# Kernel tuning notes

Measured on AMD Instinct MI355X. Metric: run time of the kernel, lower is better.

## Reference

```python
import jax, jax.numpy as jnp
import numpy as np

N = 100_000
E = 1_600_000
F_IN = 14
H = 64
N_BLOCKS = 105
N_STEMS_OUT = 105
S = 10_000
KEEP = 0.8  # 1 - drop_prob


def setup_inputs() -> dict:
    key = jax.random.key(0)
    ks = jax.random.split(key, 16)
    x = jax.random.normal(ks[0], (N, F_IN), dtype=jnp.float32)
    edge_index = jax.random.randint(ks[1], (2, E), 0, N, dtype=jnp.int64)
    stem_idxs = jax.random.randint(ks[2], (S,), 0, N, dtype=jnp.int64)
    # learned params (glorot-ish init)
    W1 = jax.random.normal(ks[3], (F_IN + 1, H), dtype=jnp.float32) / np.sqrt(F_IN + 1)
    b1 = jnp.zeros((H,), dtype=jnp.float32)
    W2 = jax.random.normal(ks[4], (H, H), dtype=jnp.float32) / np.sqrt(H)
    b2 = jnp.zeros((H,), dtype=jnp.float32)
    Wb = jax.random.normal(ks[5], (H, N_BLOCKS), dtype=jnp.float32) / np.sqrt(H)
    bb = jnp.zeros((N_BLOCKS,), dtype=jnp.float32)
    Ws = jax.random.normal(ks[6], (H, N_STEMS_OUT), dtype=jnp.float32) / np.sqrt(H)
    bs = jnp.zeros((N_STEMS_OUT,), dtype=jnp.float32)
    # inverted-dropout masks (deterministic reference for F.dropout(p=0.2))
    drop1 = (jax.random.bernoulli(ks[7], KEEP, (N, H)).astype(jnp.float32)) / KEEP
    drop2 = (jax.random.bernoulli(ks[8], KEEP, (N, H)).astype(jnp.float32)) / KEEP
    # gumbel noise g = -log(-log(U)) for gumbel_softmax(tau=1, hard=False)
    u1 = jax.random.uniform(ks[9], (N, N_BLOCKS), minval=1e-10, maxval=1.0)
    u2 = jax.random.uniform(ks[10], (N, N_STEMS_OUT), minval=1e-10, maxval=1.0)
    gb = -jnp.log(-jnp.log(u1)).astype(jnp.float32)
    gs = -jnp.log(-jnp.log(u2)).astype(jnp.float32)
    return {"x": x, "W1": W1, "b1": b1, "W2": W2, "b2": b2,
            "Wb": Wb, "bb": bb, "Ws": Ws, "bs": bs,
            "drop1": drop1, "drop2": drop2, "gb": gb, "gs": gs,
            "edge_index": edge_index, "stem_idxs": stem_idxs}


def gcn_conv(x, W, b, src, dst, norm, n):
    """PyG GCNConv (normalize=True, self-loops already appended in src/dst/norm)."""
    xw = x @ W                                    # [n, out]
    msg = xw[src] * norm[:, None]                 # gather + scale  [E+n, out]
    out = jax.ops.segment_sum(msg, dst, num_segments=n)  # scatter-add
    return out + b


def _gcn_norm(edge_index, n):
    # append self loops, edge weight 1; symmetric normalization
    loops = jnp.arange(n, dtype=edge_index.dtype)
    src = jnp.concatenate([edge_index[0], loops])
    dst = jnp.concatenate([edge_index[1], loops])
    deg = jax.ops.segment_sum(jnp.ones_like(dst, dtype=jnp.float32), dst, num_segments=n)
    dis = jnp.where(deg > 0, jax.lax.rsqrt(deg), 0.0)
    norm = dis[src] * dis[dst]
    return src, dst, norm


def reference(x, W1, b1, W2, b2, Wb, bb, Ws, bs, drop1, drop2, gb, gs, edge_index, stem_idxs):
    n = x.shape[0]
    stem_feature = jnp.zeros((n,), dtype=x.dtype).at[stem_idxs].set(1.0)
    h = jnp.concatenate([x, stem_feature[:, None]], axis=1)  # [N, F_IN+1]
    src, dst, norm = _gcn_norm(edge_index, n)
    h = jax.nn.relu(gcn_conv(h, W1, b1, src, dst, norm, n)) * drop1
    h = jax.nn.relu(gcn_conv(h, W2, b2, src, dst, norm, n)) * drop2
    block_logits = h @ Wb + bb
    stem_logits = h @ Ws + bs
    selected_block = jax.nn.softmax(block_logits + gb, axis=-1)  # gumbel_softmax tau=1 soft
    selected_stem = jax.nn.softmax(stem_logits + gs, axis=-1)
    return (block_logits, stem_logits, selected_block, selected_stem)
```

## Files before the change

kernel.cpp:

```cpp
#include <hip/hip_runtime.h>
#include <hip/hip_bf16.h>
#include <math.h>

#define N_NODES 100000
#define N_EDGES 1600000
#define FIN 14
#define H 64
#define NB 105
#define S_CNT 10000
#define SCAN_BLOCKS 391
#define NBKT 391
#define BBLK 250
#define EPB 6400

__global__ __launch_bounds__(256) void deg_kernel(const int* __restrict__ dst,
                                                  int* __restrict__ deg) {
    int e = blockIdx.x * 256 + threadIdx.x;
    atomicAdd(&deg[dst[e]], 1);
}

__global__ __launch_bounds__(256) void stem_kernel(const int* __restrict__ idx,
                                                   float* __restrict__ stem01) {
    int i = blockIdx.x * 256 + threadIdx.x;
    if (i < S_CNT) stem01[idx[i]] = 1.0f;
}

__global__ __launch_bounds__(256) void dis_kernel(const int* __restrict__ deg,
                                                  float* __restrict__ dis) {
    int i = blockIdx.x * 256 + threadIdx.x;
    if (i < N_NODES) dis[i] = rsqrtf((float)deg[i] + 1.0f);
}

__global__ __launch_bounds__(256) void scan1_kernel(const int* __restrict__ deg,
                                                    int* __restrict__ rowptr,
                                                    int* __restrict__ bsum) {
    __shared__ int s[256];
    int t = threadIdx.x;
    int i = blockIdx.x * 256 + t;
    int v = (i < N_NODES) ? deg[i] : 0;
    s[t] = v;
    __syncthreads();
#pragma unroll
    for (int o = 1; o < 256; o <<= 1) {
        int x = (t >= o) ? s[t - o] : 0;
        __syncthreads();
        s[t] += x;
        __syncthreads();
    }
    if (i < N_NODES) rowptr[i + 1] = s[t];
    if (t == 255) bsum[blockIdx.x] = s[255];
}

__global__ __launch_bounds__(512) void scan2_kernel(const int* __restrict__ bsum,
                                                    int* __restrict__ boff) {
    __shared__ int s[512];
    int t = threadIdx.x;
    int v = (t < SCAN_BLOCKS) ? bsum[t] : 0;
    s[t] = v;
    __syncthreads();
#pragma unroll
    for (int o = 1; o < 512; o <<= 1) {
        int x = (t >= o) ? s[t - o] : 0;
        __syncthreads();
        s[t] += x;
        __syncthreads();
    }
    if (t < SCAN_BLOCKS) boff[t] = s[t] - v;
}

__global__ __launch_bounds__(256) void scan3_kernel(const int* __restrict__ boff,
                                                    int* __restrict__ rowptr) {
    int t = threadIdx.x;
    int i = blockIdx.x * 256 + t;
    if (i < N_NODES) rowptr[i + 1] += boff[blockIdx.x];
    if (i == 0) rowptr[0] = 0;
}

__global__ __launch_bounds__(256) void bincnt_kernel(const int* __restrict__ dst,
                                                     int* __restrict__ hist) {
    __shared__ int lh[NBKT];
    int t = threadIdx.x;
    for (int i = t; i < NBKT; i += 256) lh[i] = 0;
    __syncthreads();
    int e0 = blockIdx.x * EPB;
    for (int i = t; i < EPB; i += 256) atomicAdd(&lh[dst[e0 + i] >> 8], 1);
    __syncthreads();
    for (int i = t; i < NBKT; i += 256) hist[i * BBLK + blockIdx.x] = lh[i];
}

__global__ __launch_bounds__(256) void binscan_kernel(int* __restrict__ hist,
                                                      const int* __restrict__ rowptr) {
    __shared__ int s[256];
    int t = threadIdx.x, b = blockIdx.x;
    int v = (t < BBLK) ? hist[b * BBLK + t] : 0;
    s[t] = v;
    __syncthreads();
#pragma unroll
    for (int o = 1; o < 256; o <<= 1) {
        int x = (t >= o) ? s[t - o] : 0;
        __syncthreads();
        s[t] += x;
        __syncthreads();
    }
    if (t < BBLK) hist[b * BBLK + t] = rowptr[b * 256] + s[t] - v;
}

__global__ __launch_bounds__(256) void binscat_kernel(const int* __restrict__ src,
                                                      const int* __restrict__ dst,
                                                      const int* __restrict__ hist,
                                                      int* __restrict__ tmp) {
    __shared__ int lofs[NBKT];
    __shared__ int lcnt[NBKT];
    int t = threadIdx.x;
    for (int i = t; i < NBKT; i += 256) {
        lofs[i] = hist[i * BBLK + blockIdx.x];
        lcnt[i] = 0;
    }
    __syncthreads();
    int e0 = blockIdx.x * EPB;
    for (int i = t; i < EPB; i += 256) {
        int s = src[e0 + i], d = dst[e0 + i];
        int b = d >> 8;
        int r = atomicAdd(&lcnt[b], 1);
        tmp[lofs[b] + r] = s | ((d & 255) << 17);
    }
}

__global__ __launch_bounds__(256) void bsort_kernel(const int* __restrict__ tmp,
                                                    const int* __restrict__ rowptr,
                                                    int* __restrict__ col) {
    __shared__ int cur[256];
    int t = threadIdx.x, b = blockIdx.x;
    int n0 = b * 256;
    int idx = n0 + t;
    cur[t] = (idx < N_NODES) ? rowptr[idx] : 0;
    __syncthreads();
    int beg = rowptr[n0];
    int nend = n0 + 256; if (nend > N_NODES) nend = N_NODES;
    int end = rowptr[nend];
    for (int i = beg + t; i < end; i += 256) {
        int p = tmp[i];
        int pos = atomicAdd(&cur[p >> 17], 1);
        col[pos] = p & 0x1FFFF;
    }
}

__global__ __launch_bounds__(256) void wpadT_kernel(const float* __restrict__ Wb,
                                                    const float* __restrict__ Ws,
                                                    float* __restrict__ WpT) {
    int i = blockIdx.x * 256 + threadIdx.x;
    if (i < 224 * 64) {
        int c = i >> 6, k = i & 63;
        float w = 0.f;
        if (c < NB) w = Wb[k * NB + c];
        else if (c >= 112 && c < 112 + NB) w = Ws[k * NB + (c - 112)];
        WpT[i] = w;
    }
}

__global__ __launch_bounds__(256) void xw1_kernel(const float* __restrict__ x,
                                                  const float* __restrict__ stem01,
                                                  const float* __restrict__ dis,
                                                  const float* __restrict__ W1,
                                                  float* __restrict__ xws) {
    __shared__ __align__(16) float W1s[15 * 64];
    __shared__ __align__(16) float xs[4][16];
    int tid = threadIdx.x;
    for (int i = tid; i < 960; i += 256) W1s[i] = W1[i];
    int n0 = blockIdx.x * 4;
    if (tid < 60) {
        int r = tid / 15, k = tid % 15;
        int n = n0 + r;
        xs[r][k] = (k < FIN) ? x[n * FIN + k] : stem01[n];
    }
    __syncthreads();
    int r = tid >> 6, f = tid & 63;
    float acc = 0.f;
#pragma unroll
    for (int k = 0; k < 15; k++) acc += xs[r][k] * W1s[k * 64 + f];
    xws[(n0 + r) * 64 + f] = acc * dis[n0 + r];
}

__global__ __launch_bounds__(256) void agg_csr_kernel(const float* __restrict__ xws,
                                                      const int* __restrict__ rowptr,
                                                      const int* __restrict__ col,
                                                      const float* __restrict__ dis,
                                                      const float* __restrict__ bias,
                                                      const float* __restrict__ drop,
                                                      float* __restrict__ hout) {
    int node = (blockIdx.x * 256 + threadIdx.x) >> 6;
    int f = threadIdx.x & 63;
    int beg = rowptr[node], end = rowptr[node + 1];
    float acc0 = xws[node * 64 + f];
    float acc1 = 0.f, acc2 = 0.f, acc3 = 0.f;
    int j = beg;
    for (; j + 4 <= end; j += 4) {
        int s0 = col[j], s1 = col[j + 1], s2 = col[j + 2], s3 = col[j + 3];
        acc0 += xws[s0 * 64 + f];
        acc1 += xws[s1 * 64 + f];
        acc2 += xws[s2 * 64 + f];
        acc3 += xws[s3 * 64 + f];
    }
    for (; j < end; j++) acc0 += xws[col[j] * 64 + f];
    float acc = (acc0 + acc1) + (acc2 + acc3);
    float r = fmaxf(fmaf(dis[node], acc, bias[f]), 0.f) * drop[node * 64 + f];
    hout[node * 64 + f] = r;
}

__global__ __launch_bounds__(256) void xw2_kernel(const float* __restrict__ h,
                                                  const float* __restrict__ dis,
                                                  const float* __restrict__ W2,
                                                  float* __restrict__ xws) {
    __shared__ __align__(16) float W2s[64 * 64];
    __shared__ __align__(16) float hsT[64 * 68];
    int tid = threadIdx.x;
    for (int i = tid; i < 4096; i += 256) W2s[i] = W2[i];
    int n0 = blockIdx.x * 64;
    for (int i = tid; i < 4096; i += 256) {
        int m = i >> 6, k = i & 63;
        int n = n0 + m;
        hsT[k * 68 + m] = (n < N_NODES) ? h[n * 64 + k] : 0.f;
    }
    __syncthreads();
    int fg = tid & 15, mg = tid >> 4;
    int f0 = fg * 4, m0 = mg * 4;
    float acc[4][4];
#pragma unroll
    for (int i = 0; i < 4; i++)
#pragma unroll
        for (int j = 0; j < 4; j++) acc[i][j] = 0.f;
    for (int k = 0; k < 64; k++) {
        float4 w = *(const float4*)&W2s[k * 64 + f0];
        float4 hv = *(const float4*)&hsT[k * 68 + m0];
        float hh[4] = {hv.x, hv.y, hv.z, hv.w};
#pragma unroll
        for (int i = 0; i < 4; i++) {
            acc[i][0] += hh[i] * w.x;
            acc[i][1] += hh[i] * w.y;
            acc[i][2] += hh[i] * w.z;
            acc[i][3] += hh[i] * w.w;
        }
    }
#pragma unroll
    for (int i = 0; i < 4; i++) {
        int n = n0 + m0 + i;
        if (n < N_NODES) {
            float ds = dis[n];
            float4 r = make_float4(acc[i][0] * ds, acc[i][1] * ds,
                                   acc[i][2] * ds, acc[i][3] * ds);
            *(float4*)&xws[n * 64 + f0] = r;
        }
    }
}

__global__ __launch_bounds__(256) void hlog_kernel(const float* __restrict__ h2,
                                                   const float* __restrict__ WpT,
                                                   const float* __restrict__ bb,
                                                   const float* __restrict__ bs,
                                                   float* __restrict__ out) {
    __shared__ __align__(16) float hl[4][8 * 64];
    const size_t NA = (size_t)N_NODES * NB;
    int tid = threadIdx.x;
    int widx = tid >> 6, lane = tid & 63;
    int wid = blockIdx.x * 4 + widx;
    int n0 = wid * 8;
    int half = lane >> 5;
    int lp = lane & 31;

    {
        const float4* src = (const float4*)(h2 + (size_t)n0 * 64);
        float4* dstp = (float4*)hl[widx];
        dstp[lane] = src[lane];
        dstp[64 + lane] = src[64 + lane];
    }

    int hoff = half * 112;
    const float* bias = half ? bs : bb;
    bool v3 = (lp + 96) < NB;
    int c3 = v3 ? (lp + 96) : 104;
    const float* w0p = WpT + (size_t)(hoff + lp) * 64;
    const float* w1p = WpT + (size_t)(hoff + lp + 32) * 64;
    const float* w2p = WpT + (size_t)(hoff + lp + 64) * 64;
    const float* w3p = WpT + (size_t)(hoff + c3) * 64;
    float bv0 = bias[lp], bv1 = bias[lp + 32], bv2 = bias[lp + 64];
    float bv3 = v3 ? bias[lp + 96] : 0.f;

    float acc[8][4];
#pragma unroll
    for (int j = 0; j < 8; j++)
#pragma unroll
        for (int r = 0; r < 4; r++) acc[j][r] = 0.f;

    const float* hw = hl[widx];
#pragma unroll 4
    for (int k4 = 0; k4 < 16; k4++) {
        float4 w0 = *(const float4*)&w0p[k4 * 4];
        float4 w1 = *(const float4*)&w1p[k4 * 4];
        float4 w2 = *(const float4*)&w2p[k4 * 4];
        float4 w3 = *(const float4*)&w3p[k4 * 4];
#pragma unroll
        for (int j = 0; j < 8; j++) {
            float4 hq = *(const float4*)&hw[j * 64 + k4 * 4];
            acc[j][0] += hq.x * w0.x + hq.y * w0.y + hq.z * w0.z + hq.w * w0.w;
            acc[j][1] += hq.x * w1.x + hq.y * w1.y + hq.z * w1.z + hq.w * w1.w;
            acc[j][2] += hq.x * w2.x + hq.y * w2.y + hq.z * w2.z + hq.w * w2.w;
            acc[j][3] += hq.x * w3.x + hq.y * w3.y + hq.z * w3.z + hq.w * w3.w;
        }
    }

    float* ob = out + (size_t)half * NA + (size_t)n0 * NB;
#pragma unroll
    for (int j = 0; j < 8; j++) {
        float* lo = ob + (size_t)j * NB;
        lo[lp] = acc[j][0] + bv0;
        lo[lp + 32] = acc[j][1] + bv1;
        lo[lp + 64] = acc[j][2] + bv2;
        if (v3) lo[lp + 96] = acc[j][3] + bv3;
    }
}

__global__ __launch_bounds__(256) void gsm_kernel(const float* __restrict__ gb,
                                                  const float* __restrict__ gs,
                                                  float* __restrict__ out) {
    const size_t NA = (size_t)N_NODES * NB;
    int wid = blockIdx.x * 4 + (threadIdx.x >> 6);
    int lane = threadIdx.x & 63;
    int n = wid >> 1;
    if (n >= N_NODES) return;
    int head = wid & 1;
    const float* L = out + (head ? NA : 0) + (size_t)n * NB;
    const float* g = (head ? gs : gb) + (size_t)n * NB;
    float z0 = L[lane] + g[lane];
    float z1 = (lane < NB - 64) ? L[lane + 64] + g[lane + 64] : -INFINITY;
    float m = fmaxf(z0, z1);
#pragma unroll
    for (int off = 32; off; off >>= 1) m = fmaxf(m, __shfl_xor(m, off));
    float e0 = __expf(z0 - m);
    float e1 = (lane < NB - 64) ? __expf(z1 - m) : 0.f;
    float s = e0 + e1;
#pragma unroll
    for (int off = 32; off; off >>= 1) s += __shfl_xor(s, off);
    float inv = 1.f / s;
    float* o = out + (2 + head) * NA + (size_t)n * NB;
    o[lane] = e0 * inv;
    if (lane < NB - 64) o[lane + 64] = e1 * inv;
}

extern "C" void kernel_launch(void* const* d_in, const int* in_sizes, int n_in,
                              void* d_out, int out_size, void* d_ws, size_t ws_size,
                              hipStream_t stream) {
    const float* x     = (const float*)d_in[0];
    const float* W1    = (const float*)d_in[1];
    const float* b1    = (const float*)d_in[2];
    const float* W2    = (const float*)d_in[3];
    const float* b2    = (const float*)d_in[4];
    const float* Wb    = (const float*)d_in[5];
    const float* bb    = (const float*)d_in[6];
    const float* Ws    = (const float*)d_in[7];
    const float* bs    = (const float*)d_in[8];
    const float* drop1 = (const float*)d_in[9];
    const float* drop2 = (const float*)d_in[10];
    const float* gb    = (const float*)d_in[11];
    const float* gs    = (const float*)d_in[12];
    const int* edge    = (const int*)d_in[13];
    const int* stem    = (const int*)d_in[14];
    float* out = (float*)d_out;

    float* A      = (float*)d_ws;
    float* B      = A + (size_t)N_NODES * 64;
    float* dis    = B + (size_t)N_NODES * 64;
    float* stem01 = dis + N_NODES;
    int*   deg    = (int*)(stem01 + N_NODES);
    int*   rowptr = deg + N_NODES;
    int*   hist   = rowptr + (N_NODES + 1);
    int*   bsum   = hist + N_NODES;
    int*   boff   = bsum + SCAN_BLOCKS;
    int*   col    = boff + SCAN_BLOCKS;
    float* WpT    = (float*)(col + N_EDGES);
    int*   tmp    = (int*)d_out;

    const int* esrc = edge;
    const int* edst = edge + N_EDGES;

    hipMemsetAsync(deg, 0, N_NODES * sizeof(int), stream);
    hipMemsetAsync(stem01, 0, N_NODES * sizeof(float), stream);

    deg_kernel<<<N_EDGES / 256, 256, 0, stream>>>(edst, deg);
    stem_kernel<<<(S_CNT + 255) / 256, 256, 0, stream>>>(stem, stem01);
    dis_kernel<<<SCAN_BLOCKS, 256, 0, stream>>>(deg, dis);
    wpadT_kernel<<<(224 * 64 + 255) / 256, 256, 0, stream>>>(Wb, Ws, WpT);

    scan1_kernel<<<SCAN_BLOCKS, 256, 0, stream>>>(deg, rowptr, bsum);
    scan2_kernel<<<1, 512, 0, stream>>>(bsum, boff);
    scan3_kernel<<<SCAN_BLOCKS, 256, 0, stream>>>(boff, rowptr);

    bincnt_kernel<<<BBLK, 256, 0, stream>>>(edst, hist);
    binscan_kernel<<<NBKT, 256, 0, stream>>>(hist, rowptr);
    binscat_kernel<<<BBLK, 256, 0, stream>>>(esrc, edst, hist, tmp);
    bsort_kernel<<<NBKT, 256, 0, stream>>>(tmp, rowptr, col);

    xw1_kernel<<<N_NODES / 4, 256, 0, stream>>>(x, stem01, dis, W1, A);
    agg_csr_kernel<<<(N_NODES * 64) / 256, 256, 0, stream>>>(A, rowptr, col, dis, b1, drop1, B);

    xw2_kernel<<<(N_NODES + 63) / 64, 256, 0, stream>>>(B, dis, W2, B);
    agg_csr_kernel<<<(N_NODES * 64) / 256, 256, 0, stream>>>(B, rowptr, col, dis, b2, drop2, A);

    hlog_kernel<<<N_NODES / 8 / 4, 256, 0, stream>>>(A, WpT, bb, bs, out);
    gsm_kernel<<<(2 * N_NODES) / 4, 256, 0, stream>>>(gb, gs, out);
}
```

Measured before the change: 729.4 us.

## Fuse logits GEMM with gumbel softmax, staging swizzled weights in LDS

Merges the output-head GEMM kernel and the gumbel-softmax kernel into one kernel that computes the logits, adds the bias and gumbel noise, and does the row softmax in registers. This removes the round trip of reading the logits back from global memory and one kernel launch. Each block now handles a single head (grid y = 2). It loads that head's padded weight matrix into shared memory with an XOR swizzle to avoid bank conflicts, instead of reading weights from global memory per lane. The cost is that every block reloads about 28KB of weights into LDS, and the node tile in LDS is staged twice, once per head.

```diff
diff --git a/kernel.cpp b/kernel.cpp
--- a/kernel.cpp
+++ b/kernel.cpp
@@ -253,19 +253,30 @@
     }
 }
 
-__global__ __launch_bounds__(256) void hlog_kernel(const float* __restrict__ h2,
-                                                   const float* __restrict__ WpT,
-                                                   const float* __restrict__ bb,
-                                                   const float* __restrict__ bs,
-                                                   float* __restrict__ out) {
+__global__ __launch_bounds__(256) void fh2_kernel(const float* __restrict__ h2,
+                                                  const float* __restrict__ WpT,
+                                                  const float* __restrict__ bb,
+                                                  const float* __restrict__ bs,
+                                                  const float* __restrict__ gb,
+                                                  const float* __restrict__ gs,
+                                                  float* __restrict__ out) {
+    __shared__ __align__(16) float Wl[112 * 64];
     __shared__ __align__(16) float hl[4][8 * 64];
     const size_t NA = (size_t)N_NODES * NB;
     int tid = threadIdx.x;
+    int head = blockIdx.y;
+
+    {
+        const float4* wsrc = (const float4*)(WpT + (size_t)head * 112 * 64);
+        for (int i = tid; i < 112 * 16; i += 256) {
+            int c = i >> 4, ch = i & 15;
+            float4 v = wsrc[i];
+            *(float4*)&Wl[(c << 6) + ((ch ^ (c & 15)) << 2)] = v;
+        }
+    }
+
     int widx = tid >> 6, lane = tid & 63;
-    int wid = blockIdx.x * 4 + widx;
-    int n0 = wid * 8;
-    int half = lane >> 5;
-    int lp = lane & 31;
+    int n0 = (blockIdx.x * 4 + widx) * 8;
 
     {
         const float4* src = (const float4*)(h2 + (size_t)n0 * 64);
@@ -273,77 +284,58 @@
         dstp[lane] = src[lane];
         dstp[64 + lane] = src[64 + lane];
     }
-
-    int hoff = half * 112;
-    const float* bias = half ? bs : bb;
-    bool v3 = (lp + 96) < NB;
-    int c3 = v3 ? (lp + 96) : 104;
-    const float* w0p = WpT + (size_t)(hoff + lp) * 64;
-    const float* w1p = WpT + (size_t)(hoff + lp + 32) * 64;
-    const float* w2p = WpT + (size_t)(hoff + lp + 64) * 64;
-    const float* w3p = WpT + (size_t)(hoff + c3) * 64;
-    float bv0 = bias[lp], bv1 = bias[lp + 32], bv2 = bias[lp + 64];
-    float bv3 = v3 ? bias[lp + 96] : 0.f;
-
-    float acc[8][4];
-#pragma unroll
-    for (int j = 0; j < 8; j++)
-#pragma unroll
-        for (int r = 0; r < 4; r++) acc[j][r] = 0.f;
+    __syncthreads();
+
+    float acc[8][2];
+#pragma unroll
+    for (int j = 0; j < 8; j++) { acc[j][0] = 0.f; acc[j][1] = 0.f; }
 
     const float* hw = hl[widx];
+    int sw = lane & 15;
+    int b0 = lane << 6;
+    int b1 = (lane + 64) << 6;
 #pragma unroll 4
     for (int k4 = 0; k4 < 16; k4++) {
-        float4 w0 = *(const float4*)&w0p[k4 * 4];
-        float4 w1 = *(const float4*)&w1p[k4 * 4];
-        float4 w2 = *(const float4*)&w2p[k4 * 4];
-        float4 w3 = *(const float4*)&w3p[k4 * 4];
+        int wo = (k4 ^ sw) << 2;
+        float4 w0 = *(const float4*)&Wl[b0 + wo];
+        float4 w1 = *(const float4*)&Wl[b1 + wo];
 #pragma unroll
         for (int j = 0; j < 8; j++) {
-            float4 hq = *(const float4*)&hw[j * 64 + k4 * 4];
+            float4 hq = *(const float4*)&hw[(j << 6) + (k4 << 2)];
             acc[j][0] += hq.x * w0.x + hq.y * w0.y + hq.z * w0.z + hq.w * w0.w;
             acc[j][1] += hq.x * w1.x + hq.y * w1.y + hq.z * w1.z + hq.w * w1.w;
-            acc[j][2] += hq.x * w2.x + hq.y * w2.y + hq.z * w2.z + hq.w * w2.w;
-            acc[j][3] += hq.x * w3.x + hq.y * w3.y + hq.z * w3.z + hq.w * w3.w;
         }
     }
 
-    float* ob = out + (size_t)half * NA + (size_t)n0 * NB;
+    bool v1 = lane < (NB - 64);
+    const float* bias = head ? bs : bb;
+    const float* g = head ? gs : gb;
+    float bv0 = bias[lane];
+    float bv1 = v1 ? bias[lane + 64] : 0.f;
+    float* obase = out + (size_t)head * NA;
 #pragma unroll
     for (int j = 0; j < 8; j++) {
-        float* lo = ob + (size_t)j * NB;
-        lo[lp] = acc[j][0] + bv0;
-        lo[lp + 32] = acc[j][1] + bv1;
-        lo[lp + 64] = acc[j][2] + bv2;
-        if (v3) lo[lp + 96] = acc[j][3] + bv3;
-    }
-}
-
-__global__ __launch_bounds__(256) void gsm_kernel(const float* __restrict__ gb,
-                                                  const float* __restrict__ gs,
-                                                  float* __restrict__ out) {
-    const size_t NA = (size_t)N_NODES * NB;
-    int wid = blockIdx.x * 4 + (threadIdx.x >> 6);
-    int lane = threadIdx.x & 63;
-    int n = wid >> 1;
-    if (n >= N_NODES) return;
-    int head = wid & 1;
-    const float* L = out + (head ? NA : 0) + (size_t)n * NB;
-    const float* g = (head ? gs : gb) + (size_t)n * NB;
-    float z0 = L[lane] + g[lane];
-    float z1 = (lane < NB - 64) ? L[lane + 64] + g[lane + 64] : -INFINITY;
-    float m = fmaxf(z0, z1);
-#pragma unroll
-    for (int off = 32; off; off >>= 1) m = fmaxf(m, __shfl_xor(m, off));
-    float e0 = __expf(z0 - m);
-    float e1 = (lane < NB - 64) ? __expf(z1 - m) : 0.f;
-    float s = e0 + e1;
-#pragma unroll
-    for (int off = 32; off; off >>= 1) s += __shfl_xor(s, off);
-    float inv = 1.f / s;
-    float* o = out + (2 + head) * NA + (size_t)n * NB;
-    o[lane] = e0 * inv;
-    if (lane < NB - 64) o[lane + 64] = e1 * inv;
+        int n = n0 + j;
+        const float* gr = g + (size_t)n * NB;
+        float l0 = acc[j][0] + bv0;
+        float l1 = acc[j][1] + bv1;
+        float z0 = l0 + gr[lane];
+        float z1 = v1 ? (l1 + gr[lane + 64]) : -INFINITY;
+        float m = fmaxf(z0, z1);
+#pragma unroll
+        for (int off = 32; off; off >>= 1) m = fmaxf(m, __shfl_xor(m, off));
+        float e0 = __expf(z0 - m);
+        float e1 = v1 ? __expf(z1 - m) : 0.f;
+        float s = e0 + e1;
+#pragma unroll
+        for (int off = 32; off; off >>= 1) s += __shfl_xor(s, off);
+        float inv = 1.f / s;
+        float* lo = obase + (size_t)n * NB;
+        float* so = lo + 2 * NA;
+        lo[lane] = l0;
+        so[lane] = e0 * inv;
+        if (v1) { lo[lane + 64] = l1; so[lane + 64] = e1 * inv; }
+    }
 }
 
 extern "C" void kernel_launch(void* const* d_in, const int* in_sizes, int n_in,
@@ -405,6 +397,5 @@
     xw2_kernel<<<(N_NODES + 63) / 64, 256, 0, stream>>>(B, dis, W2, B);
     agg_csr_kernel<<<(N_NODES * 64) / 256, 256, 0, stream>>>(B, rowptr, col, dis, b2, drop2, A);
 
-    hlog_kernel<<<N_NODES / 8 / 4, 256, 0, stream>>>(A, WpT, bb, bs, out);
-    gsm_kernel<<<(2 * N_NODES) / 4, 256, 0, stream>>>(gb, gs, out);
-}
+    fh2_kernel<<<dim3(N_NODES / 32, 2), 256, 0, stream>>>(A, WpT, bb, bs, gb, gs, out);
+}
```

Measured after the change: 711.0 us. -2.5%, faster.
